# Performance work log

Hardware: AMD Instinct MI355X
Metric: run time of the kernel (lower is better)

## Reference

```python
import jax, jax.numpy as jnp
import numpy as np

SOS_TOKEN = 1
B, H, V, T = 64, 1024, 32000, 40
INPUT_SIZE = 4096


def setup_inputs() -> dict:
    key = jax.random.key(0)
    ks = jax.random.split(key, 12)
    s = 1.0 / np.sqrt(H)
    return {
        "output": jax.random.normal(ks[0], (B, INPUT_SIZE), jnp.float32),
        "h0": jax.random.normal(ks[1], (1, B, H), jnp.float32),
        "c0": jax.random.normal(ks[2], (1, B, H), jnp.float32),
        "target_outputs": jax.random.randint(ks[3], (B, T), 0, V, jnp.int64),
        "target_lengths": jnp.full((B,), T, jnp.int64),
        "embed": jax.random.normal(ks[4], (V, H), jnp.float32),
        "w_ih": jax.random.uniform(ks[5], (4 * H, H), jnp.float32, -s, s),
        "w_hh": jax.random.uniform(ks[6], (4 * H, H), jnp.float32, -s, s),
        "b_ih": jax.random.uniform(ks[7], (4 * H,), jnp.float32, -s, s),
        "b_hh": jax.random.uniform(ks[8], (4 * H,), jnp.float32, -s, s),
        "w_out": jax.random.uniform(ks[9], (V, H), jnp.float32, -s, s),
        "b_out": jax.random.uniform(ks[10], (V,), jnp.float32, -s, s),
    }


def _lstm_cell(x, h, c, w_ih, w_hh, b_ih, b_hh):
    # PyTorch LSTMCell math; gate order i, f, g, o
    gates = x @ w_ih.T + b_ih + h @ w_hh.T + b_hh  # [B, 4H]
    i, f, g, o = jnp.split(gates, 4, axis=-1)
    c2 = jax.nn.sigmoid(f) * c + jax.nn.sigmoid(i) * jnp.tanh(g)
    h2 = jax.nn.sigmoid(o) * jnp.tanh(c2)
    return h2, c2


def reference(output, h0, c0, target_outputs, target_lengths,
              embed, w_ih, w_hh, b_ih, b_hh, w_out, b_out):
    batch = output.shape[0]
    max_lens = int(jnp.max(target_lengths))
    h, c = h0[0], c0[0]  # num_layers=1 -> [B, H]

    # Initial symbol = SOS; initial dec_o = W(embed(SOS)) (no LSTM), as in torch code
    symbol0 = jnp.full((batch,), SOS_TOKEN, dtype=target_outputs.dtype)
    dec_o0 = embed[symbol0] @ w_out.T + b_out  # [B, V]

    def step(carry, _):
        symbol, dec_o, h, c = carry
        # emit current (symbol, dec_o), then decode next
        x = embed[symbol]  # [B, H]
        h2, c2 = _lstm_cell(x, h, c, w_ih, w_hh, b_ih, b_hh)
        dec2 = h2 @ w_out.T + b_out  # [B, V]
        sym2 = jnp.argmax(dec2, axis=-1).astype(symbol.dtype)  # greedy topk(1)
        return (sym2, dec2, h2, c2), (symbol, dec_o)
    (_, _, _, _), (symbols, decs) = jax.lax.scan(
        step, (symbol0, dec_o0, h, c), None, length=max_lens)

    decoder_outs = jnp.transpose(decs, (1, 0, 2))  # [B, T, V]
    symbol_outs = jnp.transpose(symbols, (1, 0))   # [B, T]
    return decoder_outs, symbol_outs
```

## Files before the change

kernel.cpp:

```cpp
#include <hip/hip_runtime.h>

#define Bdim 64
#define Hdim 1024
#define Vdim 32000
#define Tdim 40

typedef __bf16 bf16x8 __attribute__((ext_vector_type(8)));
typedef float  f32x4  __attribute__((ext_vector_type(4)));
typedef unsigned short u16x8 __attribute__((ext_vector_type(8)));
static_assert(sizeof(bf16x8) == 16, "bf16x8 must be 16B");

__device__ __forceinline__ unsigned long long pack_key(float f, int v) {
    unsigned u = __float_as_uint(f);
    u = (u & 0x80000000u) ? ~u : (u | 0x80000000u);
    return ((unsigned long long)u << 32) | (unsigned long long)(0xFFFFFFFFu - (unsigned)v);
}

__device__ __forceinline__ int decode_key(unsigned long long key) {
    return (int)(0xFFFFFFFFu - (unsigned)(key & 0xFFFFFFFFull));
}

__device__ __forceinline__ void gll16(const void* g, void* l) {
    __builtin_amdgcn_global_load_lds(
        (const __attribute__((address_space(1))) void*)g,
        (__attribute__((address_space(3))) void*)l, 16, 0, 0);
}

struct BSplit2 { unsigned short h, m; };

__device__ __forceinline__ BSplit2 bsplit2v(float x) {
    __bf16 h = (__bf16)x;  float r = x - (float)h;
    __bf16 m = (__bf16)r;
    BSplit2 s;
    s.h = __builtin_bit_cast(unsigned short, h);
    s.m = __builtin_bit_cast(unsigned short, m);
    return s;
}

__device__ __forceinline__ void bsplit2(float x, unsigned short& a, unsigned short& b) {
    BSplit2 s = bsplit2v(x);
    a = s.h; b = s.m;
}

template<int NW, int NCH, bool ARGMAX, bool BIAS, bool GATHER, bool NTST>
__device__ __forceinline__ void mm_core(
    unsigned char* sm,
    unsigned long long (*red)[4][16],
    const float* __restrict__ W,
    const unsigned short* __restrict__ Ah,
    const unsigned short* __restrict__ Am,
    const float* __restrict__ Gsrc,
    const unsigned long long* __restrict__ slots_in, int tstep,
    float* __restrict__ sym_dst,
    int n0, const float* __restrict__ bias,
    float* __restrict__ out, size_t out_bstride,
    unsigned long long* __restrict__ slots_out)
{
    constexpr int NT     = NW * 64;
    constexpr int WBYTES = NW * 2048;
    constexpr int BUFSZ  = WBYTES + 8192;

    const int tid  = threadIdx.x;
    const int lane = tid & 63;
    const int wid  = tid >> 6;

    f32x4 acc[4] = {};

    const unsigned char* Wb = (const unsigned char*)W;
    const unsigned char* Apb[2] = {(const unsigned char*)Ah, (const unsigned char*)Am};

    const int ar = tid >> 2, as = tid & 3;
    const int aswz = as ^ ((ar >> 1) & 3);
    const size_t asrc_off = (size_t)ar * 2048 + (size_t)aswz * 16;
    const size_t aldst    = (size_t)ar * 64 + (size_t)aswz * 16;

    const float* grow = nullptr;
    if constexpr (GATHER) {
        if (tid < 256) {
            int symv = 1;
            if (tstep > 0) {
                unsigned long long key = slots_in[ar];
                symv = decode_key(key);
                if (sym_dst != nullptr && as == 0)
                    sym_dst[ar * Tdim + tstep] = (float)symv;
            }
            grow = Gsrc + (size_t)symv * 1024 + as * 8;
        }
    }

    auto stage = [&](int bufidx, int ch) {
        unsigned char* bb = sm + bufidx * BUFSZ;
        const size_t kb4 = (size_t)ch * 128;
#pragma unroll
        for (int s = 0; s < 2; s++) {
            int gg = tid + NT * s;
            int rw = gg >> 3, cc = gg & 7;
            int sg = cc ^ (rw & 7);
            gll16(Wb + (size_t)rw * 4096 + kb4 + (size_t)sg * 16,
                  bb + ((wid * 64 + NT * s) << 4));
        }
        if constexpr (GATHER) {
            if (tid < 256) {
                const float* p = grow + ch * 32;
                float4 f0 = *(const float4*)(p);
                float4 f1 = *(const float4*)(p + 4);
                u16x8 vh, vm;
                BSplit2 s0 = bsplit2v(f0.x); vh[0] = s0.h; vm[0] = s0.m;
                BSplit2 s1 = bsplit2v(f0.y); vh[1] = s1.h; vm[1] = s1.m;
                BSplit2 s2 = bsplit2v(f0.z); vh[2] = s2.h; vm[2] = s2.m;
                BSplit2 s3 = bsplit2v(f0.w); vh[3] = s3.h; vm[3] = s3.m;
                BSplit2 s4 = bsplit2v(f1.x); vh[4] = s4.h; vm[4] = s4.m;
                BSplit2 s5 = bsplit2v(f1.y); vh[5] = s5.h; vm[5] = s5.m;
                BSplit2 s6 = bsplit2v(f1.z); vh[6] = s6.h; vm[6] = s6.m;
                BSplit2 s7 = bsplit2v(f1.w); vh[7] = s7.h; vm[7] = s7.m;
                *(u16x8*)(bb + WBYTES + aldst)        = vh;
                *(u16x8*)(bb + WBYTES + 4096 + aldst) = vm;
            }
        } else {
            if (tid < 256) {
                const size_t kb2 = (size_t)ch * 64;
#pragma unroll
                for (int pl = 0; pl < 2; pl++)
                    gll16(Apb[pl] + asrc_off + kb2,
                          bb + WBYTES + pl * 4096 + (wid << 10));
            }
        }
    };

    stage(0, 0);
    __syncthreads();

    const int col  = lane & 15;
    const int kg   = lane >> 4;
    const int wrow = wid * 16 + col;
    const int wg0  = (2 * kg) ^ (wrow & 7);
    const int wg1  = (2 * kg + 1) ^ (wrow & 7);

#pragma unroll 2
    for (int ch = 0; ch < NCH; ch++) {
        if (ch + 1 < NCH) stage((ch + 1) & 1, ch + 1);
        unsigned char* base = sm + (ch & 1) * BUFSZ;

        const unsigned char* Wr = base + wrow * 128;
        f32x4 w0 = *(const f32x4*)(Wr + (wg0 << 4));
        f32x4 w1 = *(const f32x4*)(Wr + (wg1 << 4));
        bf16x8 whi, wmid;
#pragma unroll
        for (int j = 0; j < 4; j++) {
            float x0 = w0[j], x1 = w1[j];
            __bf16 a0 = (__bf16)x0; float r0 = x0 - (float)a0;
            whi[j] = a0; wmid[j] = (__bf16)r0;
            __bf16 a1 = (__bf16)x1; float r1 = x1 - (float)a1;
            whi[4 + j] = a1; wmid[4 + j] = (__bf16)r1;
        }
#pragma unroll
        for (int bt = 0; bt < 4; bt++) {
            const int arow = bt * 16 + col;
            const unsigned char* Ar = base + WBYTES + arow * 64
                                    + ((kg ^ ((arow >> 1) & 3)) << 4);
            bf16x8 ahi = *(const bf16x8*)Ar;
            bf16x8 ami = *(const bf16x8*)(Ar + 4096);
            acc[bt] = __builtin_amdgcn_mfma_f32_16x16x32_bf16(whi,  ahi, acc[bt], 0, 0, 0);
            acc[bt] = __builtin_amdgcn_mfma_f32_16x16x32_bf16(whi,  ami, acc[bt], 0, 0, 0);
            acc[bt] = __builtin_amdgcn_mfma_f32_16x16x32_bf16(wmid, ahi, acc[bt], 0, 0, 0);
        }
        __syncthreads();
    }

    const int ncol = n0 + wid * 16 + kg * 4;
    f32x4 bv = {};
    if (BIAS) bv = *(const f32x4*)(bias + ncol);

    unsigned long long bk[4];
#pragma unroll
    for (int bt = 0; bt < 4; bt++) {
        const int b = bt * 16 + col;
        float* op = out + (size_t)b * out_bstride + ncol;
        f32x4 vv;
        unsigned long long best = 0ull;
#pragma unroll
        for (int r = 0; r < 4; r++) {
            float val = acc[bt][r];
            if (BIAS) val += bv[r];
            vv[r] = val;
            if (ARGMAX) {
                unsigned long long key = pack_key(val, ncol + r);
                if (key > best) best = key;
            }
        }
        if constexpr (NTST)
            __builtin_nontemporal_store(vv, (f32x4*)op);
        else
            *(f32x4*)op = vv;
        bk[bt] = best;
    }

    if constexpr (ARGMAX) {
#pragma unroll
        for (int bt = 0; bt < 4; bt++) {
            unsigned long long k = bk[bt];
            unsigned long long o = __shfl_xor(k, 16, 64); if (o > k) k = o;
            o = __shfl_xor(k, 32, 64);                    if (o > k) k = o;
            if (lane < 16) red[wid][bt][lane] = k;
        }
        __syncthreads();
        if (tid < 64) {
            const int bt = tid >> 4, c = tid & 15;
            unsigned long long k = red[0][bt][c];
#pragma unroll
            for (int w = 1; w < NW; w++)
                if (red[w][bt][c] > k) k = red[w][bt][c];
            atomicMax(&slots_out[bt * 16 + c], k);
        }
    }
}

template<bool AM>
__global__ __launch_bounds__(512, 4) void k_combined(
    const float* __restrict__ w_out, const float* __restrict__ w_hh,
    const unsigned short* __restrict__ la_h, const unsigned short* __restrict__ la_m,
    const unsigned short* __restrict__ ga_h, const unsigned short* __restrict__ ga_m,
    const float* __restrict__ b_out, float* __restrict__ dec_out,
    float* __restrict__ gp0, unsigned long long* __restrict__ slots, int nhh)
{
    __shared__ __align__(16) unsigned char smem[2][24576];
    __shared__ unsigned long long red[8][4][16];
    const int bid = blockIdx.x;
    if (bid < nhh) {
        mm_core<8, 32, false, false, false, false>(&smem[0][0], red,
            w_hh + (size_t)bid * 131072, ga_h, ga_m, nullptr, nullptr, 0, nullptr,
            bid * 128, nullptr, gp0, 4096, nullptr);
    } else {
        const int vb = (bid - nhh) * 128;
        mm_core<8, 32, AM, true, false, true>(&smem[0][0], red,
            w_out + (size_t)vb * Hdim, la_h, la_m, nullptr, nullptr, 0, nullptr,
            vb, b_out, dec_out, (size_t)Tdim * Vdim, slots);
    }
}

__global__ __launch_bounds__(256, 2) void k_gates_ih(
    const float* __restrict__ w_ih, const float* __restrict__ embed,
    unsigned long long* __restrict__ slots, int t,
    float* __restrict__ sym_out, float* __restrict__ gp)
{
    __shared__ __align__(16) unsigned char smem[2][16384];
    const int nbi = blockIdx.x, z = blockIdx.y;
    const float* W = w_ih + (size_t)nbi * 65536 + z * 256;
    float* gout = gp + (size_t)(1 + z) * (Bdim * 4096);
    mm_core<4, 8, false, false, true, false>(&smem[0][0], nullptr, W,
        nullptr, nullptr, embed + z * 256, slots, t,
        ((nbi == 0 && z == 0) ? sym_out : nullptr),
        nbi * 64, nullptr, gout, 4096, nullptr);
}

__global__ void k_cell(const float* __restrict__ gp, const float* __restrict__ b_ih,
                       const float* __restrict__ b_hh, float* __restrict__ cbuf,
                       unsigned short* __restrict__ hh, unsigned short* __restrict__ hm,
                       unsigned long long* __restrict__ slots)
{
    const int idx = blockIdx.x * 256 + threadIdx.x;
    const int b = idx >> 10, k = idx & 1023;
    const size_t S = (size_t)Bdim * 4096;
    const size_t base = (size_t)b * 4096;
    float g[4];
#pragma unroll
    for (int q = 0; q < 4; q++) {
        size_t o = base + q * 1024 + k;
        float s = gp[o];
#pragma unroll
        for (int i = 1; i < 5; i++) s += gp[i * S + o];
        g[q] = s + b_ih[q * 1024 + k] + b_hh[q * 1024 + k];
    }
    float si = 1.f / (1.f + expf(-g[0]));
    float sf = 1.f / (1.f + expf(-g[1]));
    float so = 1.f / (1.f + expf(-g[3]));
    float c  = cbuf[idx];
    float c2 = sf * c + si * tanhf(g[2]);
    float h2 = so * tanhf(c2);
    cbuf[idx] = c2;
    unsigned short hs, ms;
    bsplit2(h2, hs, ms);
    const size_t o = (size_t)b * 1024 + k;
    hh[o] = hs; hm[o] = ms;
    if (idx < 64) slots[idx] = 0ull;
}

__global__ void k_init(const float* __restrict__ embed, const float* __restrict__ h0,
                       const float* __restrict__ c0,
                       unsigned short* __restrict__ xsh, unsigned short* __restrict__ xsm,
                       unsigned short* __restrict__ hh, unsigned short* __restrict__ hm,
                       float* __restrict__ cbuf, float* __restrict__ sym_out,
                       unsigned long long* __restrict__ slots)
{
    const int b = blockIdx.x, t4 = threadIdx.x * 4;
    if (threadIdx.x == 0) { sym_out[b * Tdim] = 1.0f; slots[b] = 0ull; }
    const size_t o = (size_t)b * 1024 + t4;
    ushort4 hi4, mi4;

    float4 e = *(const float4*)(embed + 1024 + t4);
    bsplit2(e.x, hi4.x, mi4.x);
    bsplit2(e.y, hi4.y, mi4.y);
    bsplit2(e.z, hi4.z, mi4.z);
    bsplit2(e.w, hi4.w, mi4.w);
    *(ushort4*)(xsh + o) = hi4; *(ushort4*)(xsm + o) = mi4;

    float4 hv = *(const float4*)(h0 + (size_t)b * 1024 + t4);
    bsplit2(hv.x, hi4.x, mi4.x);
    bsplit2(hv.y, hi4.y, mi4.y);
    bsplit2(hv.z, hi4.z, mi4.z);
    bsplit2(hv.w, hi4.w, mi4.w);
    *(ushort4*)(hh + o) = hi4; *(ushort4*)(hm + o) = mi4;

    float4 cv = *(const float4*)(c0 + (size_t)b * 1024 + t4);
    *(float4*)(cbuf + (size_t)b * 1024 + t4) = cv;
}

__global__ void k_symfinal(const unsigned long long* __restrict__ slots,
                           float* __restrict__ sym_out)
{
    const int b = threadIdx.x;
    sym_out[b * Tdim + (Tdim - 1)] = (float)decode_key(slots[b]);
}

extern "C" void kernel_launch(void* const* d_in, const int* in_sizes, int n_in,
                              void* d_out, int out_size, void* d_ws, size_t ws_size,
                              hipStream_t stream)
{
    const float* h0    = (const float*)d_in[1];
    const float* c0    = (const float*)d_in[2];
    const float* embed = (const float*)d_in[5];
    const float* w_ih  = (const float*)d_in[6];
    const float* w_hh  = (const float*)d_in[7];
    const float* b_ih  = (const float*)d_in[8];
    const float* b_hh  = (const float*)d_in[9];
    const float* w_out = (const float*)d_in[10];
    const float* b_out = (const float*)d_in[11];

    float* out = (float*)d_out;
    float* sym_out = out + (size_t)Bdim * Tdim * Vdim;

    unsigned short* hh  = (unsigned short*)d_ws;
    unsigned short* hm  = hh + (size_t)Bdim * 1024;
    unsigned short* xsh = hm + (size_t)Bdim * 1024;
    unsigned short* xsm = xsh + (size_t)Bdim * 1024;
    float* cbuf = (float*)(xsm + (size_t)Bdim * 1024);
    float* gp   = cbuf + (size_t)Bdim * Hdim;
    unsigned long long* slots = (unsigned long long*)(gp + 5ull * Bdim * 4096);

    k_init<<<Bdim, 256, 0, stream>>>(embed, h0, c0, xsh, xsm,
                                     hh, hm, cbuf, sym_out, slots);

    k_combined<false><<<282, 512, 0, stream>>>(w_out, w_hh, xsh, xsm, hh, hm,
                                               b_out, out, gp, slots, 32);

    for (int t = 0; t < Tdim - 1; t++) {
        k_gates_ih<<<dim3(64, 4), 256, 0, stream>>>(w_ih, embed, slots, t,
                                                    sym_out, gp);
        k_cell<<<Bdim * Hdim / 256, 256, 0, stream>>>(gp, b_ih, b_hh, cbuf,
                                                      hh, hm, slots);
        const int nhh = (t + 1 < Tdim - 1) ? 32 : 0;
        k_combined<true><<<250 + nhh, 512, 0, stream>>>(w_out, w_hh, hh, hm, hh, hm,
                                                        b_out, out + (size_t)(t + 1) * Vdim,
                                                        gp, slots, nhh);
    }
    k_symfinal<<<1, 64, 0, stream>>>(slots, sym_out);
}
```

Measured before the change: 2.282 ms.

## Fuse LSTM cell update into gates kernel via last-block-done counters

Removes the separate k_cell launch per timestep. Each k_gates_ih block bumps an atomic counter for its hidden-column group, and the last of the 16 blocks in that group runs the cell update for those 64 columns across all batches. Argmax slots are now double-buffered so the next step's slots can be cleared while the current ones are still being read. This saves 39 kernel launches and their gaps, at the cost of a serialized tail in which only 16 blocks do the cell work, plus extra fences and atomics.

Result: slower. 3.655 ms (+60.2%).

```diff
diff --git a/kernel.cpp b/kernel.cpp
--- a/kernel.cpp
+++ b/kernel.cpp
@@ -221,7 +221,7 @@
     const unsigned short* __restrict__ la_h, const unsigned short* __restrict__ la_m,
     const unsigned short* __restrict__ ga_h, const unsigned short* __restrict__ ga_m,
     const float* __restrict__ b_out, float* __restrict__ dec_out,
-    float* __restrict__ gp0, unsigned long long* __restrict__ slots, int nhh)
+    float* __restrict__ gp0, unsigned long long* __restrict__ slots_w, int nhh)
 {
     __shared__ __align__(16) unsigned char smem[2][24576];
     __shared__ unsigned long long red[8][4][16];
@@ -234,55 +234,68 @@
         const int vb = (bid - nhh) * 128;
         mm_core<8, 32, AM, true, false, true>(&smem[0][0], red,
             w_out + (size_t)vb * Hdim, la_h, la_m, nullptr, nullptr, 0, nullptr,
-            vb, b_out, dec_out, (size_t)Tdim * Vdim, slots);
+            vb, b_out, dec_out, (size_t)Tdim * Vdim, slots_w);
     }
 }
 
 __global__ __launch_bounds__(256, 2) void k_gates_ih(
     const float* __restrict__ w_ih, const float* __restrict__ embed,
-    unsigned long long* __restrict__ slots, int t,
-    float* __restrict__ sym_out, float* __restrict__ gp)
+    const unsigned long long* __restrict__ slots_cur, int t,
+    float* __restrict__ sym_out, float* __restrict__ gp,
+    const float* __restrict__ b_ih, const float* __restrict__ b_hh,
+    float* __restrict__ cbuf,
+    unsigned short* __restrict__ hh, unsigned short* __restrict__ hm,
+    unsigned long long* __restrict__ slots_next, int* __restrict__ ctr)
 {
     __shared__ __align__(16) unsigned char smem[2][16384];
+    __shared__ int s_old;
     const int nbi = blockIdx.x, z = blockIdx.y;
+    const int tid = threadIdx.x;
     const float* W = w_ih + (size_t)nbi * 65536 + z * 256;
     float* gout = gp + (size_t)(1 + z) * (Bdim * 4096);
     mm_core<4, 8, false, false, true, false>(&smem[0][0], nullptr, W,
-        nullptr, nullptr, embed + z * 256, slots, t,
+        nullptr, nullptr, embed + z * 256, slots_cur, t,
         ((nbi == 0 && z == 0) ? sym_out : nullptr),
         nbi * 64, nullptr, gout, 4096, nullptr);
-}
-
-__global__ void k_cell(const float* __restrict__ gp, const float* __restrict__ b_ih,
-                       const float* __restrict__ b_hh, float* __restrict__ cbuf,
-                       unsigned short* __restrict__ hh, unsigned short* __restrict__ hm,
-                       unsigned long long* __restrict__ slots)
-{
-    const int idx = blockIdx.x * 256 + threadIdx.x;
-    const int b = idx >> 10, k = idx & 1023;
-    const size_t S = (size_t)Bdim * 4096;
-    const size_t base = (size_t)b * 4096;
-    float g[4];
-#pragma unroll
-    for (int q = 0; q < 4; q++) {
-        size_t o = base + q * 1024 + k;
-        float s = gp[o];
-#pragma unroll
-        for (int i = 1; i < 5; i++) s += gp[i * S + o];
-        g[q] = s + b_ih[q * 1024 + k] + b_hh[q * 1024 + k];
-    }
-    float si = 1.f / (1.f + expf(-g[0]));
-    float sf = 1.f / (1.f + expf(-g[1]));
-    float so = 1.f / (1.f + expf(-g[3]));
-    float c  = cbuf[idx];
-    float c2 = sf * c + si * tanhf(g[2]);
-    float h2 = so * tanhf(c2);
-    cbuf[idx] = c2;
-    unsigned short hs, ms;
-    bsplit2(h2, hs, ms);
-    const size_t o = (size_t)b * 1024 + k;
-    hh[o] = hs; hm[o] = ms;
-    if (idx < 64) slots[idx] = 0ull;
+
+    const int grp = nbi & 15;
+    __threadfence();
+    __syncthreads();
+    if (tid == 0) s_old = atomicAdd(&ctr[grp], 1);
+    __syncthreads();
+    if (s_old == 15) {
+        __threadfence();
+        const size_t S = (size_t)Bdim * 4096;
+#pragma unroll
+        for (int i = 0; i < 16; i++) {
+            const int e = i * 256 + tid;
+            const int b = e >> 6;
+            const int k = grp * 64 + (e & 63);
+            const size_t base = (size_t)b * 4096;
+            float g[4];
+#pragma unroll
+            for (int q = 0; q < 4; q++) {
+                size_t o = base + q * 1024 + k;
+                float s = gp[o];
+#pragma unroll
+                for (int p = 1; p < 5; p++) s += gp[p * S + o];
+                g[q] = s + b_ih[q * 1024 + k] + b_hh[q * 1024 + k];
+            }
+            float si = 1.f / (1.f + expf(-g[0]));
+            float sf = 1.f / (1.f + expf(-g[1]));
+            float so = 1.f / (1.f + expf(-g[3]));
+            const int ci = b * 1024 + k;
+            float c  = cbuf[ci];
+            float c2 = sf * c + si * tanhf(g[2]);
+            float h2 = so * tanhf(c2);
+            cbuf[ci] = c2;
+            unsigned short hs, ms;
+            bsplit2(h2, hs, ms);
+            hh[ci] = hs; hm[ci] = ms;
+        }
+        if (tid < 4) slots_next[grp * 4 + tid] = 0ull;
+        if (tid == 0) atomicExch(&ctr[grp], 0);
+    }
 }
 
 __global__ void k_init(const float* __restrict__ embed, const float* __restrict__ h0,
@@ -290,10 +303,14 @@
                        unsigned short* __restrict__ xsh, unsigned short* __restrict__ xsm,
                        unsigned short* __restrict__ hh, unsigned short* __restrict__ hm,
                        float* __restrict__ cbuf, float* __restrict__ sym_out,
-                       unsigned long long* __restrict__ slots)
+                       unsigned long long* __restrict__ slots, int* __restrict__ ctr)
 {
     const int b = blockIdx.x, t4 = threadIdx.x * 4;
-    if (threadIdx.x == 0) { sym_out[b * Tdim] = 1.0f; slots[b] = 0ull; }
+    if (threadIdx.x == 0) {
+        sym_out[b * Tdim] = 1.0f;
+        slots[b] = 0ull; slots[64 + b] = 0ull;
+        if (b < 16) ctr[b] = 0;
+    }
     const size_t o = (size_t)b * 1024 + t4;
     ushort4 hi4, mi4;
 
@@ -346,22 +363,23 @@
     float* cbuf = (float*)(xsm + (size_t)Bdim * 1024);
     float* gp   = cbuf + (size_t)Bdim * Hdim;
     unsigned long long* slots = (unsigned long long*)(gp + 5ull * Bdim * 4096);
+    int* ctr = (int*)(slots + 128);
 
     k_init<<<Bdim, 256, 0, stream>>>(embed, h0, c0, xsh, xsm,
-                                     hh, hm, cbuf, sym_out, slots);
+                                     hh, hm, cbuf, sym_out, slots, ctr);
 
     k_combined<false><<<282, 512, 0, stream>>>(w_out, w_hh, xsh, xsm, hh, hm,
                                                b_out, out, gp, slots, 32);
 
     for (int t = 0; t < Tdim - 1; t++) {
-        k_gates_ih<<<dim3(64, 4), 256, 0, stream>>>(w_ih, embed, slots, t,
-                                                    sym_out, gp);
-        k_cell<<<Bdim * Hdim / 256, 256, 0, stream>>>(gp, b_ih, b_hh, cbuf,
-                                                      hh, hm, slots);
+        k_gates_ih<<<dim3(64, 4), 256, 0, stream>>>(
+            w_ih, embed, slots + (t & 1) * 64, t, sym_out, gp,
+            b_ih, b_hh, cbuf, hh, hm, slots + ((t + 1) & 1) * 64, ctr);
+
         const int nhh = (t + 1 < Tdim - 1) ? 32 : 0;
-        k_combined<true><<<250 + nhh, 512, 0, stream>>>(w_out, w_hh, hh, hm, hh, hm,
-                                                        b_out, out + (size_t)(t + 1) * Vdim,
-                                                        gp, slots, nhh);
-    }
-    k_symfinal<<<1, 64, 0, stream>>>(slots, sym_out);
-}
+        k_combined<true><<<250 + nhh, 512, 0, stream>>>(
+            w_out, w_hh, hh, hm, hh, hm, b_out, out + (size_t)(t + 1) * Vdim,
+            gp, slots + ((t + 1) & 1) * 64, nhh);
+    }
+    k_symfinal<<<1, 64, 0, stream>>>(slots + ((Tdim - 1) & 1) * 64, sym_out);
+}
```
